# Optimization experiments

Measured on AMD Instinct MI355X. Metric: run time of the kernel, lower is better.

Reference implementation:

```python
import jax, jax.numpy as jnp
import numpy as np

EPS = 1e-5
K = 3          # lisa kernel taps
GROUP = 4      # lisa groups
DILS = (3, 5, 7)


def ln4d(x, g, b):
    # LayerNormalization4D: stats over channel dim; torch uses sqrt(clamp(var, eps))
    mu = x.mean(axis=1, keepdims=True)
    var = ((x - mu) ** 2).mean(axis=1, keepdims=True)
    std = jnp.sqrt(jnp.maximum(var, EPS))
    return (x - mu) / std * g[None, :, None, None] + b[None, :, None, None]


def ln4dcf(x, g, b):
    # LayerNormalization4DCF: stats over (C, F) dims of [B,C,T,F]; sqrt(var + eps)
    mu = x.mean(axis=(1, 3), keepdims=True)
    var = ((x - mu) ** 2).mean(axis=(1, 3), keepdims=True)
    return (x - mu) / jnp.sqrt(var + EPS) * g[None, :, None, :] + b[None, :, None, :]


def prelu(x, a):
    return jnp.where(x >= 0, x, a * x)


def lisa(x, conv_w, inside_all, lamb_l, lamb_h, dilation, horizontal):
    # unfold-based local gated conv-attention
    n, c, h, w = x.shape
    pad = dilation  # = dilation * (K - 1) // 2 for K == 3
    # global avg pool -> 1x1 conv -> tanh: per-(group, tap) scalar filter
    filt = jnp.tanh(x.mean(axis=(2, 3)) @ conv_w.T).reshape(n, GROUP, K)
    # expand group weights to per-channel (channel cc belongs to group cc // (c//GROUP))
    wc = jnp.repeat(filt, c // GROUP, axis=1)  # [n, c, K]
    axis = 3 if horizontal else 2
    padw = [(0, 0)] * 4
    padw[axis] = (pad, pad)
    xp = jnp.pad(x, padw, mode='reflect')  # ReflectionPad2d
    L = w if horizontal else h
    out = jnp.zeros_like(x)
    for ki in range(K):  # fixed 3 taps: shifted-slice form of F.unfold
        sl = jax.lax.slice_in_dim(xp, ki * dilation, ki * dilation + L, axis=axis)
        out = out + sl * wc[:, :, ki][:, :, None, None]
    gap = x.mean(axis=axis, keepdims=True)  # AdaptiveAvgPool2d((None,1)) / ((1,None))
    ia = inside_all[None, :, None, None]
    out_low = (out * (ia + 1.0) - ia * gap) * lamb_l[None, :, None, None]
    return out_low + x * (lamb_h[None, :, None, None] + 1.0)


def forward(x, br_g, br_b, lisa_w, lisa_in, lisa_ll, lisa_lh, mix_gamma, mix_beta,
            convb_w, convb_b, gn_g, gn_b, convb_a,
            q_w, q_b, q_a, q_lng, q_lnb,
            k_w, k_b, k_a, k_lng, k_lnb,
            v_w, v_b, v_a, v_lng, v_lnb,
            proj_w, proj_b, proj_a, proj_lng, proj_lnb):
    B, C, T, F = x.shape
    bsum = jnp.zeros_like(x)
    for i in range(3):  # three dilation branches, each: intra (freq axis) then inter (time axis)
        b = lisa(ln4d(x, br_g[i], br_b[i]), lisa_w[i], lisa_in[i], lisa_ll[i], lisa_lh[i], DILS[i], True)
        b = lisa(ln4d(b, br_g[i + 3], br_b[i + 3]), lisa_w[i + 3], lisa_in[i + 3], lisa_ll[i + 3], lisa_lh[i + 3], DILS[i], False)
        bsum = bsum + mix_gamma[i][None, :, None, None] * b + x * mix_beta[i][None, :, None, None]
    # conv_b: 1x1 conv -> GroupNorm(1, C) -> PReLU
    y = jnp.einsum('bctf,oc->botf', bsum, convb_w) + convb_b[None, :, None, None]
    mu = y.mean(axis=(1, 2, 3), keepdims=True)
    var = ((y - mu) ** 2).mean(axis=(1, 2, 3), keepdims=True)
    y = (y - mu) / jnp.sqrt(var + EPS) * gn_g[None, :, None, None] + gn_b[None, :, None, None]
    output = prelu(y, convb_a)

    def head_proj(wt, bs, a, lng, lnb):
        # per-head 1x1 conv -> PReLU -> LN4DCF, vectorized over heads
        z = jnp.einsum('bctf,hec->hbetf', output, wt) + bs[:, None, :, None, None]
        z = prelu(z, a[:, None, None, None, None])
        mz = z.mean(axis=(2, 4), keepdims=True)
        vz = ((z - mz) ** 2).mean(axis=(2, 4), keepdims=True)
        return (z - mz) / jnp.sqrt(vz + EPS) * lng[:, None, :, None, :] + lnb[:, None, :, None, :]

    Q = head_proj(q_w, q_b, q_a, q_lng, q_lnb)   # [H,B,E,T,F]
    Kh = head_proj(k_w, k_b, k_a, k_lng, k_lnb)  # [H,B,E,T,F]
    V = head_proj(v_w, v_b, v_a, v_lng, v_lnb)   # [H,B,D,T,F]
    H, E, D = q_w.shape[0], q_w.shape[1], v_w.shape[1]
    Qm = Q.transpose(0, 1, 3, 2, 4).reshape(H, B, T, E * F)
    Km = Kh.transpose(0, 1, 3, 2, 4).reshape(H, B, T, E * F)
    Vm = V.transpose(0, 1, 3, 2, 4).reshape(H, B, T, D * F)
    scale = float(np.sqrt(E * F))
    attn = jax.nn.softmax(jnp.einsum('hbtd,hbsd->hbts', Qm, Km) / scale, axis=-1)
    o = jnp.einsum('hbts,hbsd->hbtd', attn, Vm).reshape(H, B, T, D, F)
    o = o.transpose(1, 0, 3, 2, 4).reshape(B, H * D, T, F)  # matches torch view/transpose chain
    o = prelu(jnp.einsum('bctf,oc->botf', o, proj_w) + proj_b[None, :, None, None], proj_a)
    o = ln4dcf(o, proj_lng, proj_lnb)
    return o + output


def setup_inputs():
    B, C, T, F = 4, 64, 1000, 129
    H, E, D = 4, 4, 16  # E = ceil(512/129), D = C // H
    ks = iter(jax.random.split(jax.random.key(0), 64))
    r = lambda shape, s=0.1: jax.random.normal(next(ks), shape, dtype=jnp.float32) * s
    return dict(
        x=jax.random.normal(next(ks), (B, C, T, F), dtype=jnp.float32),
        br_g=1.0 + r((6, C)), br_b=r((6, C)),
        lisa_w=r((6, GROUP * K, C)), lisa_in=r((6, C)), lisa_ll=r((6, C)), lisa_lh=r((6, C)),
        mix_gamma=r((3, C)), mix_beta=1.0 + r((3, C)),
        convb_w=r((C, C)), convb_b=r((C,)), gn_g=1.0 + r((C,)), gn_b=r((C,)),
        convb_a=jnp.asarray(0.25, jnp.float32),
        q_w=r((H, E, C)), q_b=r((H, E)), q_a=0.25 + r((H,)), q_lng=1.0 + r((H, E, F)), q_lnb=r((H, E, F)),
        k_w=r((H, E, C)), k_b=r((H, E)), k_a=0.25 + r((H,)), k_lng=1.0 + r((H, E, F)), k_lnb=r((H, E, F)),
        v_w=r((H, D, C)), v_b=r((H, D)), v_a=0.25 + r((H,)), v_lng=1.0 + r((H, D, F)), v_lnb=r((H, D, F)),
        proj_w=r((C, C)), proj_b=r((C,)), proj_a=jnp.asarray(0.25, jnp.float32),
        proj_lng=1.0 + r((C, F)), proj_lnb=r((C, F)),
    )


def reference(x, br_g, br_b, lisa_w, lisa_in, lisa_ll, lisa_lh, mix_gamma, mix_beta,
              convb_w, convb_b, gn_g, gn_b, convb_a,
              q_w, q_b, q_a, q_lng, q_lnb,
              k_w, k_b, k_a, k_lng, k_lnb,
              v_w, v_b, v_a, v_lng, v_lnb,
              proj_w, proj_b, proj_a, proj_lng, proj_lnb):
    return forward(x, br_g, br_b, lisa_w, lisa_in, lisa_ll, lisa_lh, mix_gamma, mix_beta,
                   convb_w, convb_b, gn_g, gn_b, convb_a,
                   q_w, q_b, q_a, q_lng, q_lnb,
                   k_w, k_b, k_a, k_lng, k_lnb,
                   v_w, v_b, v_a, v_lng, v_lnb,
                   proj_w, proj_b, proj_a, proj_lng, proj_lnb)
```

## Files before the change

kernel.cpp:

```cpp
#include <hip/hip_runtime.h>
#include <hip/hip_bf16.h>

#define Bz 4
#define Cc 64
#define Tt 1000
#define Ff 129
#define TF 129000
#define CTF 8256000
#define SZ 33024000L
#define EPSv 1e-5f

#define KQK 544
#define KPV 1024
#define LDP 2000
#define NV 2064

typedef __attribute__((ext_vector_type(8))) short bf16x8;
typedef __attribute__((ext_vector_type(4))) float f32x4;

__device__ __forceinline__ ushort bf_bits(__hip_bfloat16 h){
  union { __hip_bfloat16 h; ushort u; } c; c.h = h; return c.u;
}
__device__ __forceinline__ float bits_f32(ushort u){
  union { float f; unsigned int i; } c; c.i = ((unsigned int)u) << 16; return c.f;
}

__device__ __forceinline__ float wave_sum(float v){
#pragma unroll
  for (int o = 32; o; o >>= 1) v += __shfl_down(v, o, 64);
  return v;
}
__device__ __forceinline__ float wave_bcast_sum(float v){
#pragma unroll
  for (int o = 1; o < 64; o <<= 1) v += __shfl_xor(v, o, 64);
  return v;
}
__device__ __forceinline__ float blk_sum256(float v, float* red){
  __syncthreads();
  v = wave_sum(v);
  int tid = threadIdx.x;
  if ((tid & 63) == 0) red[tid >> 6] = v;
  __syncthreads();
  return red[0] + red[1] + red[2] + red[3];
}
__device__ __forceinline__ float blk_max256(float v, float* red){
  __syncthreads();
#pragma unroll
  for (int o = 32; o; o >>= 1) v = fmaxf(v, __shfl_down(v, o, 64));
  int tid = threadIdx.x;
  if ((tid & 63) == 0) red[tid >> 6] = v;
  __syncthreads();
  return fmaxf(fmaxf(red[0], red[1]), fmaxf(red[2], red[3]));
}

__global__ void k_zero(float* s){ if (threadIdx.x < 8) s[threadIdx.x] = 0.f; }

__global__ __launch_bounds__(256) void k_ln4d(const float* __restrict__ in, float* __restrict__ out,
                       const float* __restrict__ g, const float* __restrict__ be){
  int gid = blockIdx.x*256 + threadIdx.x;
  if (gid >= Bz*TF) return;
  int b = gid / TF, p = gid - b*TF;
  size_t base = (size_t)b*CTF + p;
  float v[64]; float s1 = 0.f, s2 = 0.f;
#pragma unroll
  for (int c = 0; c < 64; c++){ float x = in[base + (size_t)c*TF]; v[c] = x; s1 += x; s2 += x*x; }
  float mu = s1*(1.f/64.f);
  float var = s2*(1.f/64.f) - mu*mu;
  float rstd = rsqrtf(fmaxf(var, EPSv));
#pragma unroll
  for (int c = 0; c < 64; c++) out[base + (size_t)c*TF] = (v[c]-mu)*rstd*g[c] + be[c];
}

__global__ void k_chmean(const float* __restrict__ in, float* __restrict__ m){
  int bc = blockIdx.x;
  const float4* p = (const float4*)(in + (size_t)bc*TF);
  float s = 0.f;
  for (int i = threadIdx.x; i < TF/4; i += 256){ float4 u = p[i]; s += u.x+u.y+u.z+u.w; }
  __shared__ float red[4];
  s = blk_sum256(s, red);
  if (threadIdx.x == 0) m[bc] = s * (1.f/(float)TF);
}

__global__ void k_filt(const float* __restrict__ m, const float* __restrict__ w, float* __restrict__ filt){
  int t = threadIdx.x;
  if (t >= Bz*12) return;
  int b = t/12, gk = t - b*12;
  float s = 0.f;
  for (int c = 0; c < 64; c++) s += m[b*64+c]*w[gk*64+c];
  filt[t] = tanhf(s);
}

__global__ void k_lisa_h(const float* __restrict__ in, float* __restrict__ out,
                         const float* __restrict__ filt, const float* __restrict__ iap,
                         const float* __restrict__ llp, const float* __restrict__ lhp, int dil){
  __shared__ float r[132];
  int row = blockIdx.x;
  int c = (row / Tt) % Cc;
  int b = row / (Tt*Cc);
  size_t base = (size_t)row * Ff;
  int lane = threadIdx.x;
  float s = 0.f;
  for (int f = lane; f < Ff; f += 64){ float x = in[base+f]; r[f] = x; s += x; }
  s = wave_bcast_sum(s);
  float gap = s * (1.f/129.f);
  __syncthreads();
  int g3 = b*12 + (c>>4)*3;
  float w0 = filt[g3], w1 = filt[g3+1], w2 = filt[g3+2];
  float ia = iap[c], ll = llp[c], lh1 = lhp[c] + 1.f, ia1 = ia + 1.f;
  for (int f = lane; f < Ff; f += 64){
    int fm = f - dil; fm = fm < 0 ? -fm : fm;
    int fp = f + dil; fp = fp > 128 ? 256 - fp : fp;
    float conv = w0*r[fm] + w1*r[f] + w2*r[fp];
    out[base+f] = (conv*ia1 - ia*gap)*ll + r[f]*lh1;
  }
}

__global__ void k_colmean(const float* __restrict__ in, float* __restrict__ gapv){
  int lane = threadIdx.x & 63, strip = threadIdx.x >> 6;
  int f = blockIdx.x*64 + lane;
  int c = blockIdx.y, b = blockIdx.z;
  size_t cb = ((size_t)(b*Cc + c))*TF + f;
  float s = 0.f;
  if (f < Ff){ for (int t = strip; t < Tt; t += 4) s += in[cb + (size_t)t*Ff]; }
  __shared__ float sm[256];
  sm[threadIdx.x] = s; __syncthreads();
  if (strip == 0 && f < Ff){
    float tot = sm[threadIdx.x] + sm[threadIdx.x+64] + sm[threadIdx.x+128] + sm[threadIdx.x+192];
    gapv[(b*Cc + c)*Ff + f] = tot * (1.f/(float)Tt);
  }
}

__global__ void k_lisa_v(const float* __restrict__ in, const float* __restrict__ x,
                         float* __restrict__ A, const float* __restrict__ filt,
                         const float* __restrict__ gapv,
                         const float* __restrict__ iap, const float* __restrict__ llp,
                         const float* __restrict__ lhp,
                         const float* __restrict__ mgp, const float* __restrict__ mbp,
                         int dil, int accum){
  int lane = threadIdx.x & 63, strip = threadIdx.x >> 6;
  int ftile = blockIdx.x % 3, tch = blockIdx.x / 3;
  int f = ftile*64 + lane;
  if (f >= Ff) return;
  int c = blockIdx.y, b = blockIdx.z;
  int g3 = b*12 + (c>>4)*3;
  float w0 = filt[g3], w1 = filt[g3+1], w2 = filt[g3+2];
  float ia = iap[c], ll = llp[c], lh1 = lhp[c]+1.f, ia1 = ia+1.f;
  float mg = mgp[c], mb = mbp[c];
  float gap = gapv[(b*Cc+c)*Ff + f];
  size_t cb = ((size_t)(b*Cc + c))*TF + f;
  int tend = tch*100 + 100;
  for (int t = tch*100 + strip; t < tend; t += 4){
    int tm = t - dil; tm = tm < 0 ? -tm : tm;
    int tp = t + dil; tp = tp > 999 ? 1998 - tp : tp;
    float vm = in[cb + (size_t)tm*Ff];
    float vc = in[cb + (size_t)t*Ff];
    float vp = in[cb + (size_t)tp*Ff];
    float conv = w0*vm + w1*vc + w2*vp;
    float val = (conv*ia1 - ia*gap)*ll + vc*lh1;
    float o = mg*val + mb*x[cb + (size_t)t*Ff];
    size_t oi = cb + (size_t)t*Ff;
    A[oi] = accum ? (A[oi] + o) : o;
  }
}

__global__ __launch_bounds__(256) void k_convb(const float* __restrict__ in, float* __restrict__ out,
                        const float* __restrict__ W, const float* __restrict__ bias,
                        float* __restrict__ stat){
  __shared__ float Ws[4096];
  __shared__ float bacc[8];
  if (threadIdx.x < 8) bacc[threadIdx.x] = 0.f;
  for (int i = threadIdx.x; i < 4096; i += 256) Ws[i] = W[i];
  __syncthreads();
  int gid = blockIdx.x*256 + threadIdx.x;
  float s1 = 0.f, s2 = 0.f;
  int b = 0;
  if (gid < Bz*TF){
    b = gid / TF;
    int p = gid - b*TF;
    size_t base = (size_t)b*CTF + p;
    float v[64];
#pragma unroll
    for (int c = 0; c < 64; c++) v[c] = in[base + (size_t)c*TF];
    for (int o = 0; o < 64; o++){
      float s = bias[o];
      const float4* w4 = (const float4*)&Ws[o*64];
#pragma unroll
      for (int c = 0; c < 16; c++){
        float4 w = w4[c];
        s += v[4*c]*w.x + v[4*c+1]*w.y + v[4*c+2]*w.z + v[4*c+3]*w.w;
      }
      out[base + (size_t)o*TF] = s;
      s1 += s; s2 += s*s;
    }
  }
  int blo = __shfl(b, 0, 64), bhi = __shfl(b, 63, 64);
  if (blo == bhi){
    float w1 = wave_sum(s1), w2 = wave_sum(s2);
    if ((threadIdx.x & 63) == 0){ atomicAdd(&bacc[blo*2], w1); atomicAdd(&bacc[blo*2+1], w2); }
  } else {
    atomicAdd(&bacc[b*2], s1); atomicAdd(&bacc[b*2+1], s2);
  }
  __syncthreads();
  if (threadIdx.x < 8 && bacc[threadIdx.x] != 0.f) atomicAdd(&stat[threadIdx.x], bacc[threadIdx.x]);
}

__global__ void k_gnapply(float* __restrict__ y, const float* __restrict__ g,
                          const float* __restrict__ be, const float* __restrict__ a,
                          const float* __restrict__ stat){
  size_t gid = (size_t)blockIdx.x*256 + threadIdx.x;
  if (gid >= (size_t)(SZ/4)) return;
  size_t e0 = gid*4;
  int b = (int)(e0 / CTF);
  int c = (int)((e0 / TF) & 63);
  float mu = stat[b*2] * (1.f/(float)CTF);
  float var = stat[b*2+1] * (1.f/(float)CTF) - mu*mu;
  float rstd = rsqrtf(var + EPSv);
  float gc = g[c], bc = be[c], al = a[0];
  float4 v = *(const float4*)(y + e0);
  float o[4] = {v.x, v.y, v.z, v.w};
#pragma unroll
  for (int i = 0; i < 4; i++){
    float z = (o[i]-mu)*rstd*gc + bc;
    o[i] = z >= 0.f ? z : al*z;
  }
  *(float4*)(y + e0) = make_float4(o[0], o[1], o[2], o[3]);
}

__global__ __launch_bounds__(256) void k_qkvP(const float* __restrict__ Y,
    const float* __restrict__ qw, const float* __restrict__ qb, const float* __restrict__ qa,
    const float* __restrict__ kw, const float* __restrict__ kb, const float* __restrict__ ka,
    const float* __restrict__ vw, const float* __restrict__ vb, const float* __restrict__ va,
    __hip_bfloat16* __restrict__ Z){
  __shared__ float Ws[96*64];
  __shared__ float Bs[96], As[96];
  for (int i = threadIdx.x; i < 96*64; i += 256){
    int r = i >> 6, c = i & 63;
    float w;
    if (r < 16) w = qw[(r)*64 + c];
    else if (r < 32) w = kw[(r-16)*64 + c];
    else w = vw[(r-32)*64 + c];
    Ws[i] = w;
  }
  if (threadIdx.x < 96){
    int r = threadIdx.x;
    if (r < 16){ Bs[r] = qb[r]; As[r] = qa[r>>2]; }
    else if (r < 32){ Bs[r] = kb[r-16]; As[r] = ka[(r-16)>>2]; }
    else { Bs[r] = vb[r-32]; As[r] = va[(r-32)>>4]; }
  }
  __syncthreads();
  int gid = blockIdx.x*256 + threadIdx.x;
  if (gid >= Bz*TF) return;
  int b = gid / TF, p = gid - b*TF;
  size_t base = (size_t)b*CTF + p;
  float v[64];
#pragma unroll
  for (int c = 0; c < 64; c++) v[c] = Y[base + (size_t)c*TF];
  __hip_bfloat16* zb = Z + ((size_t)b*96)*TF + p;
  for (int r = 0; r < 96; r++){
    float s = Bs[r];
    const float4* w4 = (const float4*)&Ws[r*64];
#pragma unroll
    for (int c = 0; c < 16; c++){
      float4 w = w4[c];
      s += v[4*c]*w.x + v[4*c+1]*w.y + v[4*c+2]*w.z + v[4*c+3]*w.w;
    }
    s = s >= 0.f ? s : As[r]*s;
    zb[(size_t)r*TF] = __float2bfloat16(s);
  }
}

__global__ __launch_bounds__(256) void k_qkvN(const __hip_bfloat16* __restrict__ Z,
    const float* __restrict__ qg, const float* __restrict__ qz,
    const float* __restrict__ kg, const float* __restrict__ kz,
    const float* __restrict__ vg, const float* __restrict__ vz,
    __hip_bfloat16* __restrict__ Qm, __hip_bfloat16* __restrict__ Km,
    __hip_bfloat16* __restrict__ Vm){
  __shared__ ushort zt[96*129];
  __shared__ float ps1[256], ps2[256];
  __shared__ float mug[12], rsg[12];
  int t = blockIdx.x, b = blockIdx.y;
  const ushort* Zb = (const ushort*)(Z + ((size_t)b*96)*TF + (size_t)t*Ff);
  int tid = threadIdx.x;
  int u = tid/10, l = tid - u*10;
  int kind = 0, h = 0, jbase = 0, g = 0, rbase = 0;
  bool act = tid < 240;
  if (act){
    if (u < 4){ kind = 0; h = u; jbase = 0; g = h; rbase = h*4; }
    else if (u < 8){ kind = 1; h = u-4; jbase = 0; g = 4+h; rbase = 16+h*4; }
    else { int uv = u-8; kind = 2; h = uv>>2; jbase = (uv&3)*516; g = 8+h; rbase = 32+h*16; }
  }
  float s1 = 0.f, s2 = 0.f;
  if (act){
    for (int j = jbase + l; j < jbase + 516; j += 10){
      int e = j/129, f = j - e*129;
      int r = rbase + e;
      ushort raw = Zb[(size_t)r*TF + f];
      float z = bits_f32(raw);
      s1 += z; s2 += z*z;
      zt[r*129 + f] = raw;
    }
  }
  ps1[tid] = s1; ps2[tid] = s2;
  __syncthreads();
  if (tid < 12){
    int t0, cnt; float n;
    if (tid < 8){ t0 = tid*10; cnt = 10; n = 516.f; }
    else { t0 = (8 + (tid-8)*4)*10; cnt = 40; n = 2064.f; }
    float a = 0.f, q = 0.f;
    for (int i = 0; i < cnt; i++){ a += ps1[t0+i]; q += ps2[t0+i]; }
    float mu = a/n;
    mug[tid] = mu;
    rsg[tid] = rsqrtf(q/n - mu*mu + EPSv);
  }
  __syncthreads();
  if (act){
    float mu = mug[g], rs = rsg[g];
    size_t obase = (size_t)(h*Bz + b)*Tt + t;
    const float* lg; const float* lb; __hip_bfloat16* outp;
    if (kind == 0){ lg = qg + h*516; lb = qz + h*516; outp = Qm + obase*KQK; }
    else if (kind == 1){ lg = kg + h*516; lb = kz + h*516; outp = Km + obase*KQK; }
    else { lg = vg + h*2064; lb = vz + h*2064; outp = Vm + obase*NV; }
    for (int j = jbase + l; j < jbase + 516; j += 10){
      int e = j/129, f = j - e*129;
      int r = rbase + e;
      float z = bits_f32(zt[r*129 + f]);
      float val = (z - mu)*rs*lg[j] + lb[j];
      outp[j] = __float2bfloat16(val);
    }
  } else {
    int i0 = (tid - 240)*14;
    for (int i = i0; i < i0 + 14; i++){
      int kk = i/112, pj = i - kk*112;
      int hh = pj/28, off = 516 + (pj - hh*28);
      size_t obase = (size_t)(hh*Bz + b)*Tt + t;
      (kk ? Km : Qm)[obase*KQK + off] = __float2bfloat16(0.f);
    }
  }
}

__global__ void k_vt(const ushort* __restrict__ Vm, ushort* __restrict__ Vt){
  __shared__ ushort tile[64][72];
  int t0 = blockIdx.x*64, n0 = blockIdx.y*64, hb = blockIdx.z;
  const ushort* src = Vm + (size_t)hb*Tt*NV;
  ushort* dst = Vt + (size_t)hb*NV*KPV;
  int nl = threadIdx.x & 63, tl = threadIdx.x >> 6;
#pragma unroll
  for (int i = 0; i < 16; i++){
    int t = tl + i*4;
    int gt = t0 + t, gn = n0 + nl;
    ushort v = 0;
    if (gt < Tt && gn < NV) v = src[(size_t)gt*NV + gn];
    tile[t][nl] = v;
  }
  __syncthreads();
  int tl2 = threadIdx.x & 63, nl2 = threadIdx.x >> 6;
#pragma unroll
  for (int i = 0; i < 16; i++){
    int n = nl2 + i*4;
    int gn = n0 + n;
    if (gn < NV) dst[(size_t)gn*KPV + t0 + tl2] = tile[tl2][n];
  }
}

template<int MODE>
__global__ __launch_bounds__(256) void k_gemm(
    const ushort* __restrict__ A, int lda, long strideA,
    const ushort* __restrict__ Bt, int ldb, long strideB,
    float* __restrict__ C, long strideC,
    int M, int N, int Kc, float alpha){
  __shared__ ushort As[128*40];
  __shared__ ushort Bs[128*40];
  int hb = blockIdx.z;
  const ushort* Ab = A + (long)hb*strideA;
  const ushort* Bb = Bt + (long)hb*strideB;
  int i0 = blockIdx.y*128, j0 = blockIdx.x*128;
  int tid = threadIdx.x;
  int wave = tid >> 6, lane = tid & 63;
  int wm = (wave >> 1)*64, wn = (wave & 1)*64;
  int col16 = lane & 15, quad = lane >> 4;
  f32x4 acc[4][4] = {};
  int srow = tid >> 2;
  int scol = (tid & 3)*8;
  for (int k0 = 0; k0 < Kc; k0 += 32){
#pragma unroll
    for (int r = 0; r < 2; r++){
      int row = srow + r*64;
      int gi = i0 + row;
      float4 va = (gi < M) ? *(const float4*)(Ab + (long)gi*lda + k0 + scol)
                           : make_float4(0.f,0.f,0.f,0.f);
      *(float4*)&As[row*40 + scol] = va;
      int gj = j0 + row;
      float4 vb = (gj < N) ? *(const float4*)(Bb + (long)gj*ldb + k0 + scol)
                           : make_float4(0.f,0.f,0.f,0.f);
      *(float4*)&Bs[row*40 + scol] = vb;
    }
    __syncthreads();
    bf16x8 af[4], bfr[4];
#pragma unroll
    for (int mt = 0; mt < 4; mt++) af[mt]  = *(const bf16x8*)&As[(wm + mt*16 + col16)*40 + quad*8];
#pragma unroll
    for (int nt = 0; nt < 4; nt++) bfr[nt] = *(const bf16x8*)&Bs[(wn + nt*16 + col16)*40 + quad*8];
#pragma unroll
    for (int mt = 0; mt < 4; mt++)
#pragma unroll
      for (int nt = 0; nt < 4; nt++)
        acc[mt][nt] = __builtin_amdgcn_mfma_f32_16x16x32_bf16(af[mt], bfr[nt], acc[mt][nt], 0, 0, 0);
    __syncthreads();
  }
  if (MODE == 0){
    float* Cb = C + (long)hb*strideC;
#pragma unroll
    for (int mt = 0; mt < 4; mt++){
      int ibase = i0 + wm + mt*16 + quad*4;
#pragma unroll
      for (int nt = 0; nt < 4; nt++){
        int j = j0 + wn + nt*16 + col16;
        if (j < N){
#pragma unroll
          for (int rg = 0; rg < 4; rg++){
            int i = ibase + rg;
            if (i < M) Cb[(long)i*N + j] = acc[mt][nt][rg]*alpha;
          }
        }
      }
    }
  } else {
    int h = hb >> 2, b = hb & 3;
#pragma unroll
    for (int mt = 0; mt < 4; mt++){
      int ibase = i0 + wm + mt*16 + quad*4;
#pragma unroll
      for (int nt = 0; nt < 4; nt++){
        int n = j0 + wn + nt*16 + col16;
        if (n < NV){
          int d = n / 129, f = n - d*129;
          float* oc = C + ((long)(b*64 + h*16 + d)*Tt)*Ff + f;
#pragma unroll
          for (int rg = 0; rg < 4; rg++){
            int i = ibase + rg;
            if (i < M) oc[(long)i*Ff] = acc[mt][nt][rg];
          }
        }
      }
    }
  }
}

__global__ void k_softmax(float* __restrict__ S){
  float* row = S + (size_t)blockIdx.x * Tt;
  __hip_bfloat16* prow = (__hip_bfloat16*)row;
  int tid = threadIdx.x;
  __shared__ float red[4];
  float lv[4];
#pragma unroll
  for (int k = 0; k < 4; k++){ int idx = tid + k*256; lv[k] = (idx < Tt) ? row[idx] : -1e30f; }
  float m = fmaxf(fmaxf(lv[0], lv[1]), fmaxf(lv[2], lv[3]));
  m = blk_max256(m, red);
  float s = 0.f;
#pragma unroll
  for (int k = 0; k < 4; k++){ lv[k] = __expf(lv[k]-m); s += lv[k]; }
  s = blk_sum256(s, red);
  float inv = 1.f/s;
#pragma unroll
  for (int k = 0; k < 4; k++){
    int idx = tid + k*256;
    prow[idx] = __float2bfloat16(idx < Tt ? lv[k]*inv : 0.f);
  }
}

__global__ void k_proj(float* __restrict__ Out, const float* __restrict__ Y,
                       const float* __restrict__ W, const float* __restrict__ bias,
                       const float* __restrict__ pa, const float* __restrict__ lng,
                       const float* __restrict__ lnb){
  __shared__ float ot[64][130];
  __shared__ float Ws[4096];
  __shared__ float red[4];
  int t = blockIdx.x, b = blockIdx.y;
  size_t base = (size_t)b*CTF + (size_t)t*Ff;
  for (int i = threadIdx.x; i < 4096; i += 256) Ws[i] = W[i];
  for (int idx = threadIdx.x; idx < 64*Ff; idx += 256){
    int c = idx / Ff, f = idx - c*Ff;
    ot[c][f] = Out[base + (size_t)c*TF + f];
  }
  __syncthreads();
  float alpha = pa[0];
  float pva[17], pvb[17];
  float s1 = 0.f, s2 = 0.f;
#pragma unroll
  for (int ki = 0; ki < 17; ki++){
    int idx = threadIdx.x + ki*256;
    if (idx < 32*Ff){
      int o2 = idx / Ff, f = idx - o2*Ff;
      int o = o2*2;
      const float* wa = &Ws[o*64]; const float* wb = wa + 64;
      float sa = bias[o], sb = bias[o+1];
#pragma unroll 8
      for (int c = 0; c < 64; c++){ float v = ot[c][f]; sa += v*wa[c]; sb += v*wb[c]; }
      sa = sa >= 0.f ? sa : alpha*sa;
      sb = sb >= 0.f ? sb : alpha*sb;
      pva[ki] = sa; pvb[ki] = sb;
      s1 += sa + sb; s2 += sa*sa + sb*sb;
    }
  }
  s1 = blk_sum256(s1, red);
  s2 = blk_sum256(s2, red);
  const float n = 64.f*129.f;
  float mu = s1/n;
  float rstd = rsqrtf(s2/n - mu*mu + EPSv);
#pragma unroll
  for (int ki = 0; ki < 17; ki++){
    int idx = threadIdx.x + ki*256;
    if (idx < 32*Ff){
      int o2 = idx / Ff, f = idx - o2*Ff;
      int o = o2*2;
      float va = (pva[ki]-mu)*rstd*lng[o*Ff+f] + lnb[o*Ff+f];
      float vb = (pvb[ki]-mu)*rstd*lng[(o+1)*Ff+f] + lnb[(o+1)*Ff+f];
      Out[base + (size_t)o*TF + f]     = va + Y[base + (size_t)o*TF + f];
      Out[base + (size_t)(o+1)*TF + f] = vb + Y[base + (size_t)(o+1)*TF + f];
    }
  }
}

extern "C" void kernel_launch(void* const* d_in, const int* in_sizes, int n_in,
                              void* d_out, int out_size, void* d_ws, size_t ws_size,
                              hipStream_t stream){
  const float* x       = (const float*)d_in[0];
  const float* br_g    = (const float*)d_in[1];
  const float* br_b    = (const float*)d_in[2];
  const float* lisa_w  = (const float*)d_in[3];
  const float* lisa_in = (const float*)d_in[4];
  const float* lisa_ll = (const float*)d_in[5];
  const float* lisa_lh = (const float*)d_in[6];
  const float* mix_g   = (const float*)d_in[7];
  const float* mix_b   = (const float*)d_in[8];
  const float* convb_w = (const float*)d_in[9];
  const float* convb_b = (const float*)d_in[10];
  const float* gn_g    = (const float*)d_in[11];
  const float* gn_b    = (const float*)d_in[12];
  const float* convb_a = (const float*)d_in[13];
  const float* q_w  = (const float*)d_in[14];
  const float* q_b  = (const float*)d_in[15];
  const float* q_a  = (const float*)d_in[16];
  const float* q_lg = (const float*)d_in[17];
  const float* q_lb = (const float*)d_in[18];
  const float* k_w  = (const float*)d_in[19];
  const float* k_b  = (const float*)d_in[20];
  const float* k_a  = (const float*)d_in[21];
  const float* k_lg = (const float*)d_in[22];
  const float* k_lb = (const float*)d_in[23];
  const float* v_w  = (const float*)d_in[24];
  const float* v_b  = (const float*)d_in[25];
  const float* v_a  = (const float*)d_in[26];
  const float* v_lg = (const float*)d_in[27];
  const float* v_lb = (const float*)d_in[28];
  const float* p_w  = (const float*)d_in[29];
  const float* p_b  = (const float*)d_in[30];
  const float* p_a  = (const float*)d_in[31];
  const float* p_lg = (const float*)d_in[32];
  const float* p_lb = (const float*)d_in[33];

  float* out  = (float*)d_out;
  float* buf0 = (float*)d_ws;
  float* buf1 = buf0 + SZ;
  float* buf2 = buf1 + SZ;
  float* chm  = buf2 + SZ;
  float* filt = chm + 256;
  float* stat = filt + 64;
  float* gapv = stat + 16;

  if (ws_size < (3*(size_t)SZ + 40000)*sizeof(float)) return;

  __hip_bfloat16* Qm = (__hip_bfloat16*)buf2;
  __hip_bfloat16* Km = Qm + (size_t)16*Tt*KQK;
  __hip_bfloat16* Vm = Km + (size_t)16*Tt*KQK;
  __hip_bfloat16* Z  = (__hip_bfloat16*)buf0;
  ushort* Vt = (ushort*)buf0;
  float*  S  = buf0 + (size_t)16*NV*KPV/2;

  k_zero<<<1, 64, 0, stream>>>(stat);

  const int dils[3] = {3, 5, 7};
  for (int i = 0; i < 3; i++){
    k_ln4d<<<2016, 256, 0, stream>>>(x, buf1, br_g + i*64, br_b + i*64);
    k_chmean<<<256, 256, 0, stream>>>(buf1, chm);
    k_filt<<<1, 64, 0, stream>>>(chm, lisa_w + i*768, filt);
    k_lisa_h<<<Bz*Cc*Tt, 64, 0, stream>>>(buf1, buf2, filt, lisa_in + i*64, lisa_ll + i*64, lisa_lh + i*64, dils[i]);
    k_ln4d<<<2016, 256, 0, stream>>>(buf2, buf1, br_g + (i+3)*64, br_b + (i+3)*64);
    k_chmean<<<256, 256, 0, stream>>>(buf1, chm);
    k_filt<<<1, 64, 0, stream>>>(chm, lisa_w + (i+3)*768, filt);
    k_colmean<<<dim3(3, 64, 4), 256, 0, stream>>>(buf1, gapv);
    k_lisa_v<<<dim3(30, 64, 4), 256, 0, stream>>>(buf1, x, buf0, filt, gapv,
        lisa_in + (i+3)*64, lisa_ll + (i+3)*64, lisa_lh + (i+3)*64,
        mix_g + i*64, mix_b + i*64, dils[i], i > 0 ? 1 : 0);
  }
  k_convb<<<2016, 256, 0, stream>>>(buf0, buf1, convb_w, convb_b, stat);
  k_gnapply<<<32250, 256, 0, stream>>>(buf1, gn_g, gn_b, convb_a, stat);
  k_qkvP<<<2016, 256, 0, stream>>>(buf1, q_w, q_b, q_a, k_w, k_b, k_a, v_w, v_b, v_a, Z);
  k_qkvN<<<dim3(1000, 4), 256, 0, stream>>>(Z, q_lg, q_lb, k_lg, k_lb, v_lg, v_lb, Qm, Km, Vm);
  k_vt<<<dim3(16, 33, 16), 256, 0, stream>>>((const ushort*)Vm, Vt);
  k_gemm<0><<<dim3(8, 8, 16), 256, 0, stream>>>(
      (const ushort*)Qm, KQK, (long)Tt*KQK,
      (const ushort*)Km, KQK, (long)Tt*KQK,
      S, (long)Tt*Tt, Tt, Tt, KQK, 0.04402254531f);
  k_softmax<<<16000, 256, 0, stream>>>(S);
  k_gemm<1><<<dim3(17, 8, 16), 256, 0, stream>>>(
      (const ushort*)S, LDP, (long)Tt*LDP,
      Vt, KPV, (long)NV*KPV,
      out, 0, Tt, NV, KPV, 1.f);
  k_proj<<<dim3(1000, 4), 256, 0, stream>>>(out, buf1, p_w, p_b, p_a, p_lg, p_lb);
}
```

Measured before the change: 2.921 ms.

## Split projection into per-pixel GEMM with atomic stats and separate LN-apply pass

Replaces the per-(b,t) block projection, which staged a 64x129 tile plus weights in shared memory, with two kernels. The first is a per-pixel 1x1 conv with PReLU that accumulates per-(b,t) LayerNorm sums via wave reductions and global atomics. The second applies the normalization and the residual add. It also drops the shared-memory weight staging in convb and reads weights straight from global memory. The aim is better occupancy and coalescing, at the cost of an extra full-tensor write/read pass, a zeroing launch, and float atomics.

Result: faster. 2.830 ms (-3.1%).

```diff
diff --git a/kernel.cpp b/kernel.cpp
--- a/kernel.cpp
+++ b/kernel.cpp
@@ -53,7 +53,11 @@
   return fmaxf(fmaxf(red[0], red[1]), fmaxf(red[2], red[3]));
 }
 
-__global__ void k_zero(float* s){ if (threadIdx.x < 8) s[threadIdx.x] = 0.f; }
+__global__ void k_zero8(float* s){ if (threadIdx.x < 8) s[threadIdx.x] = 0.f; }
+__global__ void k_zerop(float* ps){
+  int i = blockIdx.x*256 + threadIdx.x;
+  if (i < 8000) ps[i] = 0.f;
+}
 
 __global__ __launch_bounds__(256) void k_ln4d(const float* __restrict__ in, float* __restrict__ out,
                        const float* __restrict__ g, const float* __restrict__ be){
@@ -166,10 +170,8 @@
 __global__ __launch_bounds__(256) void k_convb(const float* __restrict__ in, float* __restrict__ out,
                         const float* __restrict__ W, const float* __restrict__ bias,
                         float* __restrict__ stat){
-  __shared__ float Ws[4096];
   __shared__ float bacc[8];
   if (threadIdx.x < 8) bacc[threadIdx.x] = 0.f;
-  for (int i = threadIdx.x; i < 4096; i += 256) Ws[i] = W[i];
   __syncthreads();
   int gid = blockIdx.x*256 + threadIdx.x;
   float s1 = 0.f, s2 = 0.f;
@@ -183,7 +185,7 @@
     for (int c = 0; c < 64; c++) v[c] = in[base + (size_t)c*TF];
     for (int o = 0; o < 64; o++){
       float s = bias[o];
-      const float4* w4 = (const float4*)&Ws[o*64];
+      const float4* w4 = (const float4*)&W[o*64];
 #pragma unroll
       for (int c = 0; c < 16; c++){
         float4 w = w4[c];
@@ -468,56 +470,68 @@
   }
 }
 
-__global__ void k_proj(float* __restrict__ Out, const float* __restrict__ Y,
-                       const float* __restrict__ W, const float* __restrict__ bias,
-                       const float* __restrict__ pa, const float* __restrict__ lng,
-                       const float* __restrict__ lnb){
-  __shared__ float ot[64][130];
-  __shared__ float Ws[4096];
-  __shared__ float red[4];
+__global__ __launch_bounds__(256) void k_projA(const float* __restrict__ in, float* __restrict__ out,
+    const float* __restrict__ W, const float* __restrict__ bias,
+    const float* __restrict__ pa, float* __restrict__ pstat){
+  int gid = blockIdx.x*256 + threadIdx.x;
+  float s1 = 0.f, s2 = 0.f;
+  int r = 3999;
+  if (gid < Bz*TF){
+    int b = gid / TF;
+    int p = gid - b*TF;
+    r = gid / 129;
+    size_t base = (size_t)b*CTF + p;
+    float al = pa[0];
+    float v[64];
+#pragma unroll
+    for (int c = 0; c < 64; c++) v[c] = in[base + (size_t)c*TF];
+    for (int o = 0; o < 64; o++){
+      float s = bias[o];
+      const float4* w4 = (const float4*)&W[o*64];
+#pragma unroll
+      for (int c = 0; c < 16; c++){
+        float4 w = w4[c];
+        s += v[4*c]*w.x + v[4*c+1]*w.y + v[4*c+2]*w.z + v[4*c+3]*w.w;
+      }
+      s = s >= 0.f ? s : al*s;
+      out[base + (size_t)o*TF] = s;
+      s1 += s; s2 += s*s;
+    }
+  }
+  int rlo = __shfl(r, 0, 64), rhi = __shfl(r, 63, 64);
+  if (rlo == rhi){
+    float a1 = wave_sum(s1), a2 = wave_sum(s2);
+    if ((threadIdx.x & 63) == 0){
+      atomicAdd(&pstat[rlo*2], a1); atomicAdd(&pstat[rlo*2+1], a2);
+    }
+  } else {
+    bool lo = (r == rlo);
+    float a1 = wave_sum(lo ? s1 : 0.f);
+    float a2 = wave_sum(lo ? s2 : 0.f);
+    float b1 = wave_sum(lo ? 0.f : s1);
+    float b2 = wave_sum(lo ? 0.f : s2);
+    if ((threadIdx.x & 63) == 0){
+      atomicAdd(&pstat[rlo*2], a1); atomicAdd(&pstat[rlo*2+1], a2);
+      atomicAdd(&pstat[rhi*2], b1); atomicAdd(&pstat[rhi*2+1], b2);
+    }
+  }
+}
+
+__global__ __launch_bounds__(256) void k_projB(const float* __restrict__ proj,
+    const float* __restrict__ Y, float* __restrict__ Out,
+    const float* __restrict__ pstat, const float* __restrict__ lng,
+    const float* __restrict__ lnb){
   int t = blockIdx.x, b = blockIdx.y;
+  int r = b*1000 + t;
+  const float n = 64.f*129.f;
+  float mu = pstat[r*2] / n;
+  float var = pstat[r*2+1] / n - mu*mu;
+  float rstd = rsqrtf(var + EPSv);
   size_t base = (size_t)b*CTF + (size_t)t*Ff;
-  for (int i = threadIdx.x; i < 4096; i += 256) Ws[i] = W[i];
   for (int idx = threadIdx.x; idx < 64*Ff; idx += 256){
     int c = idx / Ff, f = idx - c*Ff;
-    ot[c][f] = Out[base + (size_t)c*TF + f];
-  }
-  __syncthreads();
-  float alpha = pa[0];
-  float pva[17], pvb[17];
-  float s1 = 0.f, s2 = 0.f;
-#pragma unroll
-  for (int ki = 0; ki < 17; ki++){
-    int idx = threadIdx.x + ki*256;
-    if (idx < 32*Ff){
-      int o2 = idx / Ff, f = idx - o2*Ff;
-      int o = o2*2;
-      const float* wa = &Ws[o*64]; const float* wb = wa + 64;
-      float sa = bias[o], sb = bias[o+1];
-#pragma unroll 8
-      for (int c = 0; c < 64; c++){ float v = ot[c][f]; sa += v*wa[c]; sb += v*wb[c]; }
-      sa = sa >= 0.f ? sa : alpha*sa;
-      sb = sb >= 0.f ? sb : alpha*sb;
-      pva[ki] = sa; pvb[ki] = sb;
-      s1 += sa + sb; s2 += sa*sa + sb*sb;
-    }
-  }
-  s1 = blk_sum256(s1, red);
-  s2 = blk_sum256(s2, red);
-  const float n = 64.f*129.f;
-  float mu = s1/n;
-  float rstd = rsqrtf(s2/n - mu*mu + EPSv);
-#pragma unroll
-  for (int ki = 0; ki < 17; ki++){
-    int idx = threadIdx.x + ki*256;
-    if (idx < 32*Ff){
-      int o2 = idx / Ff, f = idx - o2*Ff;
-      int o = o2*2;
-      float va = (pva[ki]-mu)*rstd*lng[o*Ff+f] + lnb[o*Ff+f];
-      float vb = (pvb[ki]-mu)*rstd*lng[(o+1)*Ff+f] + lnb[(o+1)*Ff+f];
-      Out[base + (size_t)o*TF + f]     = va + Y[base + (size_t)o*TF + f];
-      Out[base + (size_t)(o+1)*TF + f] = vb + Y[base + (size_t)(o+1)*TF + f];
-    }
+    size_t off = base + (size_t)c*TF + f;
+    Out[off] = (proj[off]-mu)*rstd*lng[idx] + lnb[idx] + Y[off];
   }
 }
 
@@ -567,6 +581,7 @@
   float* filt = chm + 256;
   float* stat = filt + 64;
   float* gapv = stat + 16;
+  float* pstat = gapv;
 
   if (ws_size < (3*(size_t)SZ + 40000)*sizeof(float)) return;
 
@@ -577,7 +592,7 @@
   ushort* Vt = (ushort*)buf0;
   float*  S  = buf0 + (size_t)16*NV*KPV/2;
 
-  k_zero<<<1, 64, 0, stream>>>(stat);
+  k_zero8<<<1, 64, 0, stream>>>(stat);
 
   const int dils[3] = {3, 5, 7};
   for (int i = 0; i < 3; i++){
@@ -607,5 +622,7 @@
       (const ushort*)S, LDP, (long)Tt*LDP,
       Vt, KPV, (long)NV*KPV,
       out, 0, Tt, NV, KPV, 1.f);
-  k_proj<<<dim3(1000, 4), 256, 0, stream>>>(out, buf1, p_w, p_b, p_a, p_lg, p_lb);
-}
+  k_zerop<<<32, 256, 0, stream>>>(pstat);
+  k_projA<<<2016, 256, 0, stream>>>(out, buf0, p_w, p_b, p_a, pstat);
+  k_projB<<<dim3(1000, 4), 256, 0, stream>>>(buf0, buf1, out, pstat, p_lg, p_lb);
+}
```
